# Kernel optimization log

Hardware: AMD Instinct MI355X
Metric: run time of the kernel (lower is better)

## Reference

```python
import jax, jax.numpy as jnp
import numpy as np

NUM_F = 5
POLY = 3
GRID_LO, GRID_HI = -1.0, 1.0


def _ext_grid():
    # 6-point grid on [-1, 1], extended by POLY knots on each side (pykan B_batch extend)
    g = np.linspace(GRID_LO, GRID_HI, NUM_F + 1)
    h = (GRID_HI - GRID_LO) / NUM_F
    left = g[0] - h * np.arange(POLY, 0, -1)
    right = g[-1] + h * np.arange(1, POLY + 1)
    return jnp.asarray(np.concatenate([left, g, right]), dtype=jnp.float32)  # (12,)


def bspline_basis(x, grid, k):
    # Cox-de Boor recursion; x: (...,), grid: (G,) shared knots -> (..., G-1-k)
    x1 = x[..., None]
    B = ((x1 >= grid[:-1]) & (x1 < grid[1:])).astype(x.dtype)
    for d in range(1, k + 1):
        left = (x1 - grid[:-(d + 1)]) / (grid[d:-1] - grid[:-(d + 1)])
        right = (grid[d + 1:] - x1) / (grid[d + 1:] - grid[1:-d])
        B = left * B[..., :-1] + right * B[..., 1:]
    return B


def setup_inputs():
    key = jax.random.key(0)
    ks = jax.random.split(key, 5)
    batch, heads, patches, dim, out_dim = 8, 4, 64, 8, 8
    act_in = heads * patches * dim    # 2048
    act_out = heads * patches * out_dim  # 2048
    N = act_in * act_out              # 4_194_304 spline edges
    C = NUM_F + POLY                  # 8 coefficients per edge
    return {
        "q": jax.random.normal(ks[0], (batch, heads, patches, dim), jnp.float32),
        "k": jax.random.normal(ks[1], (batch, heads, patches, dim), jnp.float32),
        "coef_q": jax.random.normal(ks[2], (N, C), jnp.float32) * 0.05,
        "coef_k": jax.random.normal(ks[3], (N, C), jnp.float32) * 0.05,
        "scale_base": jnp.ones((N,), jnp.float32),
        "scale_sp": jnp.ones((N,), jnp.float32),
        "mask_q": jnp.ones((N,), jnp.float32),
        "mask_k": jnp.ones((N,), jnp.float32),
        "bias_w": jax.random.normal(ks[4], (2048,), jnp.float32) * 0.02,
    }


def reference(q, k, coef_q, coef_k, scale_base, scale_sp, mask_q, mask_k, bias_w):
    batch, heads, patches, dim = q.shape
    act_in = heads * patches * dim
    act_out = bias_w.shape[0]
    out_dim = act_out // (heads * patches)
    C = NUM_F + POLY
    grid = _ext_grid()

    xq = q.reshape(batch, act_in)
    xk = k.reshape(batch, act_in)
    Bq = bspline_basis(xq, grid, POLY)  # (batch, act_in, C)
    Bk = bspline_basis(xk, grid, POLY)

    def branch(x, B, coef, mask):
        # edge activation f[o,i](x_i) = mask*(scale_base*silu(x_i) + scale_sp*spline_{o,i}(x_i)),
        # reduced over all act_in inputs -> (batch, act_out)
        sb = (mask * scale_base).reshape(act_out, act_in)
        sp = (mask * scale_sp).reshape(act_out, act_in)
        base = jax.nn.silu(x)  # (batch, act_in)
        y = jnp.einsum('bi,oi->bo', base, sb)
        y = y + jnp.einsum('bic,oic,oi->bo', B, coef.reshape(act_out, act_in, C), sp)
        return y

    y = branch(xq, Bq, coef_q, mask_q) + branch(xk, Bk, coef_k, mask_k)
    y = y.reshape(batch, heads, patches, out_dim) + bias_w.reshape(1, heads, patches, out_dim)
    return jax.nn.softmax(y, axis=-1)
```

## Files before the change

kernel.cpp:

```cpp
#include <hip/hip_runtime.h>
#include <math.h>


#define ACT 2048
#define BATCH 8
#define IBLK 64
#define NIC (ACT / IBLK)
#define OBLK 64
#define NOC (ACT / OBLK)

#define SBAR_PIN_DS() __builtin_amdgcn_sched_barrier(0x7F)

typedef float v2f __attribute__((ext_vector_type(2)));

__device__ __forceinline__ v2f fma2(v2f a, v2f b, v2f c) {
  return __builtin_elementwise_fma(a, b, c);
}
__device__ __forceinline__ v2f shflx2(v2f v, int m) {
  v2f r;
  r.x = __shfl_xor(v.x, m);
  r.y = __shfl_xor(v.y, m);
  return r;
}

__global__ void kan_precompute(const float* __restrict__ q, const float* __restrict__ k,
                               float4* __restrict__ Bq, float4* __restrict__ Bk,
                               float* __restrict__ baseq, float* __restrict__ basek) {
  int tid = blockIdx.x * blockDim.x + threadIdx.x;
  if (tid >= ACT * BATCH) return;
  int il = tid & (IBLK - 1);
  int b = (tid >> 6) & 7;
  int ic = tid >> 9;
  int i = ic * IBLK + il;
  const float t0 = -2.2f;
  const float h = 0.4f;
  for (int br = 0; br < 2; ++br) {
    const float* xsrc = br ? k : q;
    float4* Bdst = br ? Bk : Bq;
    float* basedst = br ? basek : baseq;
    float x = xsrc[(size_t)b * ACT + i];
    float Bv[11];
#pragma unroll
    for (int j = 0; j < 11; ++j) {
      float tj = t0 + h * (float)j;
      float tj1 = t0 + h * (float)(j + 1);
      Bv[j] = (x >= tj && x < tj1) ? 1.0f : 0.0f;
    }
#pragma unroll
    for (int d = 1; d <= 3; ++d) {
      float inv = 1.0f / (h * (float)d);
#pragma unroll
      for (int j = 0; j + d < 11; ++j) {
        float tj = t0 + h * (float)j;
        float tjd1 = t0 + h * (float)(j + d + 1);
        Bv[j] = (x - tj) * inv * Bv[j] + (tjd1 - x) * inv * Bv[j + 1];
      }
    }
    Bdst[((size_t)ic * 16 + b * 2 + 0) * IBLK + il] = make_float4(Bv[0], Bv[1], Bv[2], Bv[3]);
    Bdst[((size_t)ic * 16 + b * 2 + 1) * IBLK + il] = make_float4(Bv[4], Bv[5], Bv[6], Bv[7]);
    basedst[((size_t)ic * 8 + b) * IBLK + il] = x / (1.0f + expf(-x));
  }
}

__global__ __launch_bounds__(256) void kan_main(
    const float* __restrict__ coef_q, const float* __restrict__ coef_k,
    const float* __restrict__ scale_base, const float* __restrict__ scale_sp,
    const float* __restrict__ mask_q, const float* __restrict__ mask_k,
    const float4* __restrict__ Bq, const float4* __restrict__ Bk,
    const float* __restrict__ baseq, const float* __restrict__ basek,
    float* __restrict__ y_part) {
  __shared__ float4 BsQ[16 * IBLK];
  __shared__ float4 BsK[16 * IBLK];
  __shared__ float basQ[8 * IBLK];
  __shared__ float basK[8 * IBLK];

  const int t = threadIdx.x;
  const int l = t & 63;
  const int w = t >> 6;
  const int oc = blockIdx.x >> 5;
  const int ic = blockIdx.x & 31;
  const int o0 = oc * OBLK;
  const size_t ibase = (size_t)ic * IBLK + l;

  {
    const float4* srcq = Bq + (size_t)ic * 16 * IBLK;
    const float4* srck = Bk + (size_t)ic * 16 * IBLK;
#pragma unroll
    for (int r = 0; r < 4; ++r) {
      BsQ[r * 256 + t] = srcq[r * 256 + t];
      BsK[r * 256 + t] = srck[r * 256 + t];
    }
    if (t < 128) {
      reinterpret_cast<float4*>(basQ)[t] =
          reinterpret_cast<const float4*>(baseq + (size_t)ic * 8 * IBLK)[t];
    } else {
      reinterpret_cast<float4*>(basK)[t - 128] =
          reinterpret_cast<const float4*>(basek + (size_t)ic * 8 * IBLK)[t - 128];
    }
  }
  __syncthreads();

  float4 cqA[4], ckA[4], cqB[4], ckB[4];
  float scA[8], scB[8];

#define LOAD(BUF, S)                                                          \
  {                                                                           \
    const int oa_ = o0 + w * 16 + (S) * 2;                                    \
    const size_t e0_ = (size_t)oa_ * ACT + ibase;                             \
    const size_t e1_ = e0_ + ACT;                                             \
    const float4* p0 = reinterpret_cast<const float4*>(coef_q + e0_ * 8);     \
    const float4* p1 = reinterpret_cast<const float4*>(coef_q + e1_ * 8);     \
    cq##BUF[0] = p0[0]; cq##BUF[1] = p0[1];                                   \
    cq##BUF[2] = p1[0]; cq##BUF[3] = p1[1];                                   \
    const float4* r0 = reinterpret_cast<const float4*>(coef_k + e0_ * 8);     \
    const float4* r1 = reinterpret_cast<const float4*>(coef_k + e1_ * 8);     \
    ck##BUF[0] = r0[0]; ck##BUF[1] = r0[1];                                   \
    ck##BUF[2] = r1[0]; ck##BUF[3] = r1[1];                                   \
    sc##BUF[0] = mask_q[e0_];     sc##BUF[1] = mask_q[e1_];                   \
    sc##BUF[2] = mask_k[e0_];     sc##BUF[3] = mask_k[e1_];                   \
    sc##BUF[4] = scale_base[e0_]; sc##BUF[5] = scale_base[e1_];               \
    sc##BUF[6] = scale_sp[e0_];   sc##BUF[7] = scale_sp[e1_];                 \
  }

#define COMPUTE(BUF, S)                                                       \
  {                                                                           \
    const int oa_ = o0 + w * 16 + (S) * 2;                                    \
    v2f vbq = {sc##BUF[0] * sc##BUF[4], sc##BUF[1] * sc##BUF[5]};             \
    v2f vbk = {sc##BUF[2] * sc##BUF[4], sc##BUF[3] * sc##BUF[5]};             \
    v2f vsq = {sc##BUF[0] * sc##BUF[6], sc##BUF[1] * sc##BUF[7]};             \
    v2f vsk = {sc##BUF[2] * sc##BUF[6], sc##BUF[3] * sc##BUF[7]};             \
    v2f acc2[BATCH];                                                          \
    _Pragma("unroll") for (int b = 0; b < BATCH; ++b)                         \
        acc2[b] = (v2f){0.0f, 0.0f};                                          \
    v2f cs[8];                                                                \
    cs[0] = (v2f){cq##BUF[0].x, cq##BUF[2].x} * vsq;                          \
    cs[1] = (v2f){cq##BUF[0].y, cq##BUF[2].y} * vsq;                          \
    cs[2] = (v2f){cq##BUF[0].z, cq##BUF[2].z} * vsq;                          \
    cs[3] = (v2f){cq##BUF[0].w, cq##BUF[2].w} * vsq;                          \
    cs[4] = (v2f){cq##BUF[1].x, cq##BUF[3].x} * vsq;                          \
    cs[5] = (v2f){cq##BUF[1].y, cq##BUF[3].y} * vsq;                          \
    cs[6] = (v2f){cq##BUF[1].z, cq##BUF[3].z} * vsq;                          \
    cs[7] = (v2f){cq##BUF[1].w, cq##BUF[3].w} * vsq;                          \
    _Pragma("unroll") for (int b = 0; b < BATCH; ++b) {                       \
      const float4 B0 = BsQ[(b * 2 + 0) * IBLK + l];                          \
      const float4 B1 = BsQ[(b * 2 + 1) * IBLK + l];                          \
      const float bs = basQ[b * IBLK + l];                                    \
      v2f a = acc2[b];                                                        \
      a = fma2(cs[0], (v2f){B0.x, B0.x}, a);                                  \
      a = fma2(cs[1], (v2f){B0.y, B0.y}, a);                                  \
      a = fma2(cs[2], (v2f){B0.z, B0.z}, a);                                  \
      a = fma2(cs[3], (v2f){B0.w, B0.w}, a);                                  \
      a = fma2(cs[4], (v2f){B1.x, B1.x}, a);                                  \
      a = fma2(cs[5], (v2f){B1.y, B1.y}, a);                                  \
      a = fma2(cs[6], (v2f){B1.z, B1.z}, a);                                  \
      a = fma2(cs[7], (v2f){B1.w, B1.w}, a);                                  \
      a = fma2(vbq, (v2f){bs, bs}, a);                                        \
      acc2[b] = a;                                                            \
      SBAR_PIN_DS();                                                          \
    }                                                                         \
    cs[0] = (v2f){ck##BUF[0].x, ck##BUF[2].x} * vsk;                          \
    cs[1] = (v2f){ck##BUF[0].y, ck##BUF[2].y} * vsk;                          \
    cs[2] = (v2f){ck##BUF[0].z, ck##BUF[2].z} * vsk;                          \
    cs[3] = (v2f){ck##BUF[0].w, ck##BUF[2].w} * vsk;                          \
    cs[4] = (v2f){ck##BUF[1].x, ck##BUF[3].x} * vsk;                          \
    cs[5] = (v2f){ck##BUF[1].y, ck##BUF[3].y} * vsk;                          \
    cs[6] = (v2f){ck##BUF[1].z, ck##BUF[3].z} * vsk;                          \
    cs[7] = (v2f){ck##BUF[1].w, ck##BUF[3].w} * vsk;                          \
    _Pragma("unroll") for (int b = 0; b < BATCH; ++b) {                       \
      const float4 B0 = BsK[(b * 2 + 0) * IBLK + l];                          \
      const float4 B1 = BsK[(b * 2 + 1) * IBLK + l];                          \
      const float bs = basK[b * IBLK + l];                                    \
      v2f a = acc2[b];                                                        \
      a = fma2(cs[0], (v2f){B0.x, B0.x}, a);                                  \
      a = fma2(cs[1], (v2f){B0.y, B0.y}, a);                                  \
      a = fma2(cs[2], (v2f){B0.z, B0.z}, a);                                  \
      a = fma2(cs[3], (v2f){B0.w, B0.w}, a);                                  \
      a = fma2(cs[4], (v2f){B1.x, B1.x}, a);                                  \
      a = fma2(cs[5], (v2f){B1.y, B1.y}, a);                                  \
      a = fma2(cs[6], (v2f){B1.z, B1.z}, a);                                  \
      a = fma2(cs[7], (v2f){B1.w, B1.w}, a);                                  \
      a = fma2(vbk, (v2f){bs, bs}, a);                                        \
      acc2[b] = a;                                                            \
      SBAR_PIN_DS();                                                          \
    }                                                                         \
          \
    v2f n0, n1, n2, n3;                                                       \
    {                                                                         \
      const bool hi = (l & 1);                                                \
      v2f s0 = hi ? acc2[0] : acc2[4];                                        \
      v2f s1 = hi ? acc2[1] : acc2[5];                                        \
      v2f s2 = hi ? acc2[2] : acc2[6];                                        \
      v2f s3 = hi ? acc2[3] : acc2[7];                                        \
      v2f k0 = hi ? acc2[4] : acc2[0];                                        \
      v2f k1 = hi ? acc2[5] : acc2[1];                                        \
      v2f k2 = hi ? acc2[6] : acc2[2];                                        \
      v2f k3 = hi ? acc2[7] : acc2[3];                                        \
      n0 = k0 + shflx2(s0, 1);                                                \
      n1 = k1 + shflx2(s1, 1);                                                \
      n2 = k2 + shflx2(s2, 1);                                                \
      n3 = k3 + shflx2(s3, 1);                                                \
    }                                                                         \
    v2f m0, m1;                                                               \
    {                                                                         \
      const bool hi = (l & 2);                                                \
      v2f s0 = hi ? n0 : n2;                                                  \
      v2f s1 = hi ? n1 : n3;                                                  \
      v2f k0 = hi ? n2 : n0;                                                  \
      v2f k1 = hi ? n3 : n1;                                                  \
      m0 = k0 + shflx2(s0, 2);                                                \
      m1 = k1 + shflx2(s1, 2);                                                \
    }                                                                         \
    v2f r;                                                                    \
    {                                                                         \
      const bool hi = (l & 4);                                                \
      v2f s0 = hi ? m0 : m1;                                                  \
      v2f k0 = hi ? m1 : m0;                                                  \
      r = k0 + shflx2(s0, 4);                                                 \
    }                                                                         \
    r = r + shflx2(r, 8);                                                     \
    r = r + shflx2(r, 16);                                                    \
    r = r + shflx2(r, 32);                                                    \
    if (l < 8) {                                                              \
      y_part[(size_t)oa_ * (NIC * 8) + ic * 8 + l] = r.x;                     \
      y_part[(size_t)(oa_ + 1) * (NIC * 8) + ic * 8 + l] = r.y;               \
    }                                                                         \
  }

  LOAD(A, 0)
#pragma unroll 1
  for (int ss = 0; ss < 4; ++ss) {
    const int s0 = ss * 2;
    LOAD(B, s0 + 1)
    COMPUTE(A, s0)
    if (ss < 3) LOAD(A, s0 + 2)
    COMPUTE(B, s0 + 1)
  }
#undef LOAD
#undef COMPUTE
}

__global__ void kan_softmax(const float* __restrict__ y_part,
                            const float* __restrict__ bias,
                            float* __restrict__ out) {
  const int t = threadIdx.x;
  const int wid = blockIdx.x * 4 + (t >> 6);
  const int b = wid >> 8;
  const int grp = wid & 255;
  const int l = t & 63;
  const int op = l >> 3;
  const int sub = l & 7;
  const int o = grp * 8 + op;
  const int slot = ((b & 1) << 2) | (b & 2) | ((b >> 2) & 1);

  float p = 0.0f;
#pragma unroll
  for (int j = 0; j < 4; ++j) {
    int icc = sub + 8 * j;
    p += y_part[(size_t)o * (NIC * 8) + icc * 8 + slot];
  }
#pragma unroll
  for (int off = 1; off < 8; off <<= 1) p += __shfl_xor(p, off);
  float v = p + bias[o];
  float m = v;
#pragma unroll
  for (int off = 8; off < 64; off <<= 1) m = fmaxf(m, __shfl_xor(m, off));
  float e = expf(v - m);
  float ssum = e;
#pragma unroll
  for (int off = 8; off < 64; off <<= 1) ssum += __shfl_xor(ssum, off);
  if (sub == 0) out[(size_t)b * ACT + o] = e / ssum;
}

extern "C" void kernel_launch(void* const* d_in, const int* in_sizes, int n_in,
                              void* d_out, int out_size, void* d_ws, size_t ws_size,
                              hipStream_t stream) {
  const float* q          = (const float*)d_in[0];
  const float* k          = (const float*)d_in[1];
  const float* coef_q     = (const float*)d_in[2];
  const float* coef_k     = (const float*)d_in[3];
  const float* scale_base = (const float*)d_in[4];
  const float* scale_sp   = (const float*)d_in[5];
  const float* mask_q     = (const float*)d_in[6];
  const float* mask_k     = (const float*)d_in[7];
  const float* bias_w     = (const float*)d_in[8];
  float* out = (float*)d_out;

  float* ws     = (float*)d_ws;
  float* y_part = ws;
  float* Bq     = ws + 524288;
  float* Bk     = Bq + 131072;
  float* baseq  = Bk + 131072;
  float* basek  = baseq + 16384;

  kan_precompute<<<dim3(64), dim3(256), 0, stream>>>(
      q, k, (float4*)Bq, (float4*)Bk, baseq, basek);
  kan_main<<<dim3(NOC * NIC), dim3(256), 0, stream>>>(
      coef_q, coef_k, scale_base, scale_sp, mask_q, mask_k,
      (const float4*)Bq, (const float4*)Bk, baseq, basek, y_part);
  kan_softmax<<<dim3(512), dim3(256), 0, stream>>>(y_part, bias_w, out);
}
```

Baseline: 76.43 us.

## Accumulate over four input chunks per block and shrink partial-sum buffer

Each block now covers 16 outputs and walks four 64-wide input chunks in sequence, keeping two register accumulator sets across chunks instead of writing one partial per chunk. This cuts the partial-sum buffer by a factor of four and lets the softmax read one partial per lane rather than summing four. In exchange the double-buffered coefficient prefetch is dropped, so global loads are no longer overlapped with compute, and each chunk adds shared-memory reloads and barriers. Block count and output tile size per block change as well.

```diff
diff --git a/kernel.cpp b/kernel.cpp
--- a/kernel.cpp
+++ b/kernel.cpp
@@ -5,9 +5,9 @@
 #define ACT 2048
 #define BATCH 8
 #define IBLK 64
-#define NIC (ACT / IBLK)
-#define OBLK 64
-#define NOC (ACT / OBLK)
+#define NCH 4
+#define NICB 8
+#define NOB 128
 
 #define SBAR_PIN_DS() __builtin_amdgcn_sched_barrier(0x7F)
 
@@ -77,75 +77,43 @@
   const int t = threadIdx.x;
   const int l = t & 63;
   const int w = t >> 6;
-  const int oc = blockIdx.x >> 5;
-  const int ic = blockIdx.x & 31;
-  const int o0 = oc * OBLK;
-  const size_t ibase = (size_t)ic * IBLK + l;
-
-  {
-    const float4* srcq = Bq + (size_t)ic * 16 * IBLK;
-    const float4* srck = Bk + (size_t)ic * 16 * IBLK;
-#pragma unroll
-    for (int r = 0; r < 4; ++r) {
-      BsQ[r * 256 + t] = srcq[r * 256 + t];
-      BsK[r * 256 + t] = srck[r * 256 + t];
-    }
-    if (t < 128) {
-      reinterpret_cast<float4*>(basQ)[t] =
-          reinterpret_cast<const float4*>(baseq + (size_t)ic * 8 * IBLK)[t];
-    } else {
-      reinterpret_cast<float4*>(basK)[t - 128] =
-          reinterpret_cast<const float4*>(basek + (size_t)ic * 8 * IBLK)[t - 128];
-    }
-  }
-  __syncthreads();
-
-  float4 cqA[4], ckA[4], cqB[4], ckB[4];
-  float scA[8], scB[8];
-
-#define LOAD(BUF, S)                                                          \
+  const int ob = blockIdx.x >> 3;
+  const int icb = blockIdx.x & 7;
+  const int oA = ob * 16 + w * 4;
+
+  v2f accA[BATCH], accB[BATCH];
+#pragma unroll
+  for (int b = 0; b < BATCH; ++b) {
+    accA[b] = (v2f){0.0f, 0.0f};
+    accB[b] = (v2f){0.0f, 0.0f};
+  }
+
+  float4 cq[4], ck[4];
+  float sc[8];
+
+#define LOADP(O, E)                                                           \
   {                                                                           \
-    const int oa_ = o0 + w * 16 + (S) * 2;                                    \
-    const size_t e0_ = (size_t)oa_ * ACT + ibase;                             \
+    const size_t e0_ = (size_t)(O)*ACT + (E);                                 \
     const size_t e1_ = e0_ + ACT;                                             \
     const float4* p0 = reinterpret_cast<const float4*>(coef_q + e0_ * 8);     \
     const float4* p1 = reinterpret_cast<const float4*>(coef_q + e1_ * 8);     \
-    cq##BUF[0] = p0[0]; cq##BUF[1] = p0[1];                                   \
-    cq##BUF[2] = p1[0]; cq##BUF[3] = p1[1];                                   \
+    cq[0] = p0[0]; cq[1] = p0[1]; cq[2] = p1[0]; cq[3] = p1[1];               \
     const float4* r0 = reinterpret_cast<const float4*>(coef_k + e0_ * 8);     \
     const float4* r1 = reinterpret_cast<const float4*>(coef_k + e1_ * 8);     \
-    ck##BUF[0] = r0[0]; ck##BUF[1] = r0[1];                                   \
-    ck##BUF[2] = r1[0]; ck##BUF[3] = r1[1];                                   \
-    sc##BUF[0] = mask_q[e0_];     sc##BUF[1] = mask_q[e1_];                   \
-    sc##BUF[2] = mask_k[e0_];     sc##BUF[3] = mask_k[e1_];                   \
-    sc##BUF[4] = scale_base[e0_]; sc##BUF[5] = scale_base[e1_];               \
-    sc##BUF[6] = scale_sp[e0_];   sc##BUF[7] = scale_sp[e1_];                 \
-  }
-
-#define COMPUTE(BUF, S)                                                       \
+    ck[0] = r0[0]; ck[1] = r0[1]; ck[2] = r1[0]; ck[3] = r1[1];               \
+    sc[0] = mask_q[e0_];     sc[1] = mask_q[e1_];                             \
+    sc[2] = mask_k[e0_];     sc[3] = mask_k[e1_];                             \
+    sc[4] = scale_base[e0_]; sc[5] = scale_base[e1_];                         \
+    sc[6] = scale_sp[e0_];   sc[7] = scale_sp[e1_];                           \
+  }
+
+#define PHASE(ACC, CS0, CS1, BS, BAS, VB)                                     \
   {                                                                           \
-    const int oa_ = o0 + w * 16 + (S) * 2;                                    \
-    v2f vbq = {sc##BUF[0] * sc##BUF[4], sc##BUF[1] * sc##BUF[5]};             \
-    v2f vbk = {sc##BUF[2] * sc##BUF[4], sc##BUF[3] * sc##BUF[5]};             \
-    v2f vsq = {sc##BUF[0] * sc##BUF[6], sc##BUF[1] * sc##BUF[7]};             \
-    v2f vsk = {sc##BUF[2] * sc##BUF[6], sc##BUF[3] * sc##BUF[7]};             \
-    v2f acc2[BATCH];                                                          \
-    _Pragma("unroll") for (int b = 0; b < BATCH; ++b)                         \
-        acc2[b] = (v2f){0.0f, 0.0f};                                          \
-    v2f cs[8];                                                                \
-    cs[0] = (v2f){cq##BUF[0].x, cq##BUF[2].x} * vsq;                          \
-    cs[1] = (v2f){cq##BUF[0].y, cq##BUF[2].y} * vsq;                          \
-    cs[2] = (v2f){cq##BUF[0].z, cq##BUF[2].z} * vsq;                          \
-    cs[3] = (v2f){cq##BUF[0].w, cq##BUF[2].w} * vsq;                          \
-    cs[4] = (v2f){cq##BUF[1].x, cq##BUF[3].x} * vsq;                          \
-    cs[5] = (v2f){cq##BUF[1].y, cq##BUF[3].y} * vsq;                          \
-    cs[6] = (v2f){cq##BUF[1].z, cq##BUF[3].z} * vsq;                          \
-    cs[7] = (v2f){cq##BUF[1].w, cq##BUF[3].w} * vsq;                          \
     _Pragma("unroll") for (int b = 0; b < BATCH; ++b) {                       \
-      const float4 B0 = BsQ[(b * 2 + 0) * IBLK + l];                          \
-      const float4 B1 = BsQ[(b * 2 + 1) * IBLK + l];                          \
-      const float bs = basQ[b * IBLK + l];                                    \
-      v2f a = acc2[b];                                                        \
+      const float4 B0 = BS[(b * 2 + 0) * IBLK + l];                           \
+      const float4 B1 = BS[(b * 2 + 1) * IBLK + l];                           \
+      const float bs = BAS[b * IBLK + l];                                     \
+      v2f a = ACC[b];                                                         \
       a = fma2(cs[0], (v2f){B0.x, B0.x}, a);                                  \
       a = fma2(cs[1], (v2f){B0.y, B0.y}, a);                                  \
       a = fma2(cs[2], (v2f){B0.z, B0.z}, a);                                  \
@@ -154,47 +122,107 @@
       a = fma2(cs[5], (v2f){B1.y, B1.y}, a);                                  \
       a = fma2(cs[6], (v2f){B1.z, B1.z}, a);                                  \
       a = fma2(cs[7], (v2f){B1.w, B1.w}, a);                                  \
-      a = fma2(vbq, (v2f){bs, bs}, a);                                        \
-      acc2[b] = a;                                                            \
+      a = fma2(VB, (v2f){bs, bs}, a);                                         \
+      ACC[b] = a;                                                             \
       SBAR_PIN_DS();                                                          \
     }                                                                         \
-    cs[0] = (v2f){ck##BUF[0].x, ck##BUF[2].x} * vsk;                          \
-    cs[1] = (v2f){ck##BUF[0].y, ck##BUF[2].y} * vsk;                          \
-    cs[2] = (v2f){ck##BUF[0].z, ck##BUF[2].z} * vsk;                          \
-    cs[3] = (v2f){ck##BUF[0].w, ck##BUF[2].w} * vsk;                          \
-    cs[4] = (v2f){ck##BUF[1].x, ck##BUF[3].x} * vsk;                          \
-    cs[5] = (v2f){ck##BUF[1].y, ck##BUF[3].y} * vsk;                          \
-    cs[6] = (v2f){ck##BUF[1].z, ck##BUF[3].z} * vsk;                          \
-    cs[7] = (v2f){ck##BUF[1].w, ck##BUF[3].w} * vsk;                          \
-    _Pragma("unroll") for (int b = 0; b < BATCH; ++b) {                       \
-      const float4 B0 = BsK[(b * 2 + 0) * IBLK + l];                          \
-      const float4 B1 = BsK[(b * 2 + 1) * IBLK + l];                          \
-      const float bs = basK[b * IBLK + l];                                    \
-      v2f a = acc2[b];                                                        \
-      a = fma2(cs[0], (v2f){B0.x, B0.x}, a);                                  \
-      a = fma2(cs[1], (v2f){B0.y, B0.y}, a);                                  \
-      a = fma2(cs[2], (v2f){B0.z, B0.z}, a);                                  \
-      a = fma2(cs[3], (v2f){B0.w, B0.w}, a);                                  \
-      a = fma2(cs[4], (v2f){B1.x, B1.x}, a);                                  \
-      a = fma2(cs[5], (v2f){B1.y, B1.y}, a);                                  \
-      a = fma2(cs[6], (v2f){B1.z, B1.z}, a);                                  \
-      a = fma2(cs[7], (v2f){B1.w, B1.w}, a);                                  \
-      a = fma2(vbk, (v2f){bs, bs}, a);                                        \
-      acc2[b] = a;                                                            \
-      SBAR_PIN_DS();                                                          \
-    }                                                                         \
-          \
+  }
+
+#pragma unroll 1
+  for (int c = 0; c < NCH; ++c) {
+    if (c) __syncthreads();
+    const int ic = icb * NCH + c;
+    {
+      const float4* srcq = Bq + (size_t)ic * 16 * IBLK;
+      const float4* srck = Bk + (size_t)ic * 16 * IBLK;
+#pragma unroll
+      for (int r = 0; r < 4; ++r) {
+        BsQ[r * 256 + t] = srcq[r * 256 + t];
+        BsK[r * 256 + t] = srck[r * 256 + t];
+      }
+      if (t < 128) {
+        reinterpret_cast<float4*>(basQ)[t] =
+            reinterpret_cast<const float4*>(baseq + (size_t)ic * 8 * IBLK)[t];
+      } else {
+        reinterpret_cast<float4*>(basK)[t - 128] =
+            reinterpret_cast<const float4*>(basek + (size_t)ic * 8 * IBLK)[t - 128];
+      }
+    }
+    __syncthreads();
+
+    const size_t ibase = (size_t)ic * IBLK + l;
+    v2f cs[8], vb;
+
+    LOADP(oA, ibase)
+    {
+      v2f vsq = {sc[0] * sc[6], sc[1] * sc[7]};
+      vb = (v2f){sc[0] * sc[4], sc[1] * sc[5]};
+      cs[0] = (v2f){cq[0].x, cq[2].x} * vsq;
+      cs[1] = (v2f){cq[0].y, cq[2].y} * vsq;
+      cs[2] = (v2f){cq[0].z, cq[2].z} * vsq;
+      cs[3] = (v2f){cq[0].w, cq[2].w} * vsq;
+      cs[4] = (v2f){cq[1].x, cq[3].x} * vsq;
+      cs[5] = (v2f){cq[1].y, cq[3].y} * vsq;
+      cs[6] = (v2f){cq[1].z, cq[3].z} * vsq;
+      cs[7] = (v2f){cq[1].w, cq[3].w} * vsq;
+    }
+    PHASE(accA, , , BsQ, basQ, vb)
+    {
+      v2f vsk = {sc[2] * sc[6], sc[3] * sc[7]};
+      vb = (v2f){sc[2] * sc[4], sc[3] * sc[5]};
+      cs[0] = (v2f){ck[0].x, ck[2].x} * vsk;
+      cs[1] = (v2f){ck[0].y, ck[2].y} * vsk;
+      cs[2] = (v2f){ck[0].z, ck[2].z} * vsk;
+      cs[3] = (v2f){ck[0].w, ck[2].w} * vsk;
+      cs[4] = (v2f){ck[1].x, ck[3].x} * vsk;
+      cs[5] = (v2f){ck[1].y, ck[3].y} * vsk;
+      cs[6] = (v2f){ck[1].z, ck[3].z} * vsk;
+      cs[7] = (v2f){ck[1].w, ck[3].w} * vsk;
+    }
+    PHASE(accA, , , BsK, basK, vb)
+
+    LOADP(oA + 2, ibase)
+    {
+      v2f vsq = {sc[0] * sc[6], sc[1] * sc[7]};
+      vb = (v2f){sc[0] * sc[4], sc[1] * sc[5]};
+      cs[0] = (v2f){cq[0].x, cq[2].x} * vsq;
+      cs[1] = (v2f){cq[0].y, cq[2].y} * vsq;
+      cs[2] = (v2f){cq[0].z, cq[2].z} * vsq;
+      cs[3] = (v2f){cq[0].w, cq[2].w} * vsq;
+      cs[4] = (v2f){cq[1].x, cq[3].x} * vsq;
+      cs[5] = (v2f){cq[1].y, cq[3].y} * vsq;
+      cs[6] = (v2f){cq[1].z, cq[3].z} * vsq;
+      cs[7] = (v2f){cq[1].w, cq[3].w} * vsq;
+    }
+    PHASE(accB, , , BsQ, basQ, vb)
+    {
+      v2f vsk = {sc[2] * sc[6], sc[3] * sc[7]};
+      vb = (v2f){sc[2] * sc[4], sc[3] * sc[5]};
+      cs[0] = (v2f){ck[0].x, ck[2].x} * vsk;
+      cs[1] = (v2f){ck[0].y, ck[2].y} * vsk;
+      cs[2] = (v2f){ck[0].z, ck[2].z} * vsk;
+      cs[3] = (v2f){ck[0].w, ck[2].w} * vsk;
+      cs[4] = (v2f){ck[1].x, ck[3].x} * vsk;
+      cs[5] = (v2f){ck[1].y, ck[3].y} * vsk;
+      cs[6] = (v2f){ck[1].z, ck[3].z} * vsk;
+      cs[7] = (v2f){ck[1].w, ck[3].w} * vsk;
+    }
+    PHASE(accB, , , BsK, basK, vb)
+  }
+
+#define FOLD_STORE(ACC, OA)                                                   \
+  {                                                                           \
     v2f n0, n1, n2, n3;                                                       \
     {                                                                         \
       const bool hi = (l & 1);                                                \
-      v2f s0 = hi ? acc2[0] : acc2[4];                                        \
-      v2f s1 = hi ? acc2[1] : acc2[5];                                        \
-      v2f s2 = hi ? acc2[2] : acc2[6];                                        \
-      v2f s3 = hi ? acc2[3] : acc2[7];                                        \
-      v2f k0 = hi ? acc2[4] : acc2[0];                                        \
-      v2f k1 = hi ? acc2[5] : acc2[1];                                        \
-      v2f k2 = hi ? acc2[6] : acc2[2];                                        \
-      v2f k3 = hi ? acc2[7] : acc2[3];                                        \
+      v2f s0 = hi ? ACC[0] : ACC[4];                                          \
+      v2f s1 = hi ? ACC[1] : ACC[5];                                          \
+      v2f s2 = hi ? ACC[2] : ACC[6];                                          \
+      v2f s3 = hi ? ACC[3] : ACC[7];                                          \
+      v2f k0 = hi ? ACC[4] : ACC[0];                                          \
+      v2f k1 = hi ? ACC[5] : ACC[1];                                          \
+      v2f k2 = hi ? ACC[6] : ACC[2];                                          \
+      v2f k3 = hi ? ACC[7] : ACC[3];                                          \
       n0 = k0 + shflx2(s0, 1);                                                \
       n1 = k1 + shflx2(s1, 1);                                                \
       n2 = k2 + shflx2(s2, 1);                                                \
@@ -221,22 +249,16 @@
     r = r + shflx2(r, 16);                                                    \
     r = r + shflx2(r, 32);                                                    \
     if (l < 8) {                                                              \
-      y_part[(size_t)oa_ * (NIC * 8) + ic * 8 + l] = r.x;                     \
-      y_part[(size_t)(oa_ + 1) * (NIC * 8) + ic * 8 + l] = r.y;               \
-    }                                                                         \
-  }
-
-  LOAD(A, 0)
-#pragma unroll 1
-  for (int ss = 0; ss < 4; ++ss) {
-    const int s0 = ss * 2;
-    LOAD(B, s0 + 1)
-    COMPUTE(A, s0)
-    if (ss < 3) LOAD(A, s0 + 2)
-    COMPUTE(B, s0 + 1)
-  }
-#undef LOAD
-#undef COMPUTE
+      y_part[(size_t)(OA)*64 + icb * 8 + l] = r.x;                            \
+      y_part[(size_t)((OA) + 1) * 64 + icb * 8 + l] = r.y;                    \
+    }                                                                         \
+  }
+
+  FOLD_STORE(accA, oA)
+  FOLD_STORE(accB, oA + 2)
+#undef LOADP
+#undef PHASE
+#undef FOLD_STORE
 }
 
 __global__ void kan_softmax(const float* __restrict__ y_part,
@@ -252,12 +274,7 @@
   const int o = grp * 8 + op;
   const int slot = ((b & 1) << 2) | (b & 2) | ((b >> 2) & 1);
 
-  float p = 0.0f;
-#pragma unroll
-  for (int j = 0; j < 4; ++j) {
-    int icc = sub + 8 * j;
-    p += y_part[(size_t)o * (NIC * 8) + icc * 8 + slot];
-  }
+  float p = y_part[(size_t)o * 64 + sub * 8 + slot];
 #pragma unroll
   for (int off = 1; off < 8; off <<= 1) p += __shfl_xor(p, off);
   float v = p + bias[o];
@@ -287,14 +304,14 @@
 
   float* ws     = (float*)d_ws;
   float* y_part = ws;
-  float* Bq     = ws + 524288;
+  float* Bq     = ws + 131072;
   float* Bk     = Bq + 131072;
   float* baseq  = Bk + 131072;
   float* basek  = baseq + 16384;
 
   kan_precompute<<<dim3(64), dim3(256), 0, stream>>>(
       q, k, (float4*)Bq, (float4*)Bk, baseq, basek);
-  kan_main<<<dim3(NOC * NIC), dim3(256), 0, stream>>>(
+  kan_main<<<dim3(NOB * NICB), dim3(256), 0, stream>>>(
       coef_q, coef_k, scale_base, scale_sp, mask_q, mask_k,
       (const float4*)Bq, (const float4*)Bk, baseq, basek, y_part);
   kan_softmax<<<dim3(512), dim3(256), 0, stream>>>(y_part, bias_w, out);
```

Result: slower. 79.25 us (+3.7%).
